# Kernel optimization log

Measured on AMD Instinct MI355X. Metric: run time of the kernel, lower is better.

Reference implementation:

```python
import jax, jax.numpy as jnp
import numpy as np

P_DIMS = [100, 100, 80, 60, 60]
P = sum(P_DIMS)  # 400
N_STREAMS = len(P_DIMS)
MEM_ITERS = 5
DECAY = 0.8
LR = 0.5        # hebbian_learning_rate
FORGET = 0.9999 # hebbian_forget_rate
NEG_SLOPE = 0.01


def _build_masks():
    idx = np.cumsum([0] + P_DIMS)
    hier = np.zeros((P, P), np.float32)
    for i in range(N_STREAMS):
        for j in range(i, N_STREAMS):
            hier[idx[i]:idx[i + 1], idx[j]:idx[j + 1]] = 1.0
    iters = [MEM_ITERS - f for f in range(N_STREAMS)]  # [5,4,3,2,1]
    rmasks = np.zeros((MEM_ITERS, P), np.float32)
    for it in range(MEM_ITERS):
        for s, r in enumerate(iters):
            if it < r:
                rmasks[it, idx[s]:idx[s + 1]] = 1.0
    return jnp.asarray(hier), jnp.asarray(rmasks)


def setup_inputs() -> dict:
    key = jax.random.key(0)
    k1, k2, k3, k4 = jax.random.split(key, 4)
    B = 512
    return {
        'M_prev': jax.random.normal(k1, (B, P, P), dtype=jnp.float32) * 0.1,
        'p_inferred': jax.random.normal(k2, (B, P), dtype=jnp.float32),
        'p_generated': jax.random.normal(k3, (B, P), dtype=jnp.float32),
        'query': jax.random.normal(k4, (B, P), dtype=jnp.float32),
    }


def reference(M_prev, p_inferred, p_generated, query):
    hier_mask, retrieval_masks = _build_masks()

    # Hebbian update: M = clamp(forget*M_prev + lr*(p-phat)(p+phat)^T, -1, 1) * hier_mask
    outer = (p_inferred - p_generated)[:, :, None] * (p_inferred + p_generated)[:, None, :]
    M = jnp.clip(FORGET * M_prev + LR * outer, -1.0, 1.0) * hier_mask

    # Hierarchical attractor retrieval
    h = jax.nn.leaky_relu(jnp.clip(query, -1.0, 1.0), NEG_SLOPE)

    def step(h, mask):
        mv = jnp.einsum('bpq,bq->bp', M, h)
        upd = jax.nn.leaky_relu(jnp.clip(DECAY * h + mv, -1.0, 1.0), NEG_SLOPE)
        return (1.0 - mask) * h + mask * upd, None

    h, _ = jax.lax.scan(step, h, retrieval_masks)
    return h
```

## Files before the change

kernel.cpp:

```cpp
#include <hip/hip_runtime.h>


#define PDIM 400
#define FORGET 0.9999f
#define LRATE  0.5f
#define DECAY  0.8f
#define SLOPE  0.01f

__device__ __forceinline__ float leaky_clip(float x) {
    x = fminf(fmaxf(x, -1.0f), 1.0f);
    return x > 0.0f ? x : SLOPE * x;
}
__device__ __forceinline__ float clamp1(float x) {
    return fminf(fmaxf(x, -1.0f), 1.0f);
}

__device__ __forceinline__ int c4beg(int p) {
    return (p < 100) ? 0 : (p < 200) ? 25 : (p < 280) ? 50 : (p < 340) ? 70 : 85;
}

__device__ __forceinline__ float wave_sum(float x) {
    x += __int_as_float(__builtin_amdgcn_update_dpp(0, __float_as_int(x), 0xB1,  0xf, 0xf, true));
    x += __int_as_float(__builtin_amdgcn_update_dpp(0, __float_as_int(x), 0x4E,  0xf, 0xf, true));
    x += __int_as_float(__builtin_amdgcn_update_dpp(0, __float_as_int(x), 0x141, 0xf, 0xf, true));
    x += __int_as_float(__builtin_amdgcn_update_dpp(0, __float_as_int(x), 0x140, 0xf, 0xf, true));
    x += __int_as_float(__builtin_amdgcn_update_dpp(0, __float_as_int(x), 0x142, 0xf, 0xf, true));
    x += __int_as_float(__builtin_amdgcn_update_dpp(0, __float_as_int(x), 0x143, 0xf, 0xf, true));
    return __int_as_float(__builtin_amdgcn_readlane(__float_as_int(x), 63));
}

__global__ __launch_bounds__(512, 4)
void hier_mem_kernel(const float* __restrict__ M_prev,
                     const float* __restrict__ p_inf,
                     const float* __restrict__ p_gen,
                     const float* __restrict__ query,
                     float* __restrict__ out)
{
    __shared__ float s_h[2][PDIM];
    __shared__ float s_la[PDIM];

    const int b   = blockIdx.x;
    const int tid = threadIdx.x;
    const int l   = tid & 63;
    const int wid = tid >> 6;
    const float* __restrict__ Mb = M_prev + (size_t)b * PDIM * PDIM;

    if (tid < PDIM) {
        const float pi = p_inf[b * PDIM + tid];
        const float pg = p_gen[b * PDIM + tid];
        s_la[tid]   = LRATE * (pi - pg);
        s_h[0][tid] = leaky_clip(query[b * PDIM + tid]);
    }

    const float4 z4 = make_float4(0.f, 0.f, 0.f, 0.f);
    const float4* __restrict__ pi4 = (const float4*)(p_inf + (size_t)b * PDIM);
    const float4* __restrict__ pg4 = (const float4*)(p_gen + (size_t)b * PDIM);
    float4 bA, bB = z4;
    {
        const float4 x = pi4[l], y = pg4[l];
        bA = make_float4(x.x + y.x, x.y + y.y, x.z + y.z, x.w + y.w);
        if (l < 36) {
            const float4 u = pi4[64 + l], v = pg4[64 + l];
            bB = make_float4(u.x + v.x, u.y + v.y, u.z + v.z, u.w + v.w);
        }
    }
    __syncthreads();

    const int Rt[5] = {400, 340, 280, 200, 100};
    int cur = 0;

    #pragma unroll
    for (int t = 0; t < 5; ++t) {
        const int R = Rt[t];
        const float* __restrict__ hcur = s_h[cur];
        float* __restrict__ hnew = s_h[cur ^ 1];

        float4 hA = *(const float4*)(hcur + 4 * l);
        float4 hB = z4;
        if (l < 36) hB = *(const float4*)(hcur + 256 + 4 * l);

        int p = wid;
        int c4 = 0;
        float4 cA = z4, cB = z4;
        if (p < R) {
            c4 = c4beg(p);
            const float* __restrict__ row = Mb + (size_t)p * PDIM;
            if (l >= c4)               cA = *(const float4*)(row + 4 * l);
            if (l < 36 && 64 + l >= c4) cB = *(const float4*)(row + 256 + 4 * l);
        }
        while (p < R) {
            const int pn = p + 8;
            int c4n = 0;
            float4 nA = z4, nB = z4;
            if (pn < R) {
                c4n = c4beg(pn);
                const float* __restrict__ rn = Mb + (size_t)pn * PDIM;
                if (l >= c4n)                nA = *(const float4*)(rn + 4 * l);
                if (l < 36 && 64 + l >= c4n) nB = *(const float4*)(rn + 256 + 4 * l);
            }

            const float la = s_la[p];
            float acc = 0.f;
            if (l >= c4) {
                float m0 = clamp1(fmaf(FORGET, cA.x, la * bA.x));
                float m1 = clamp1(fmaf(FORGET, cA.y, la * bA.y));
                float m2 = clamp1(fmaf(FORGET, cA.z, la * bA.z));
                float m3 = clamp1(fmaf(FORGET, cA.w, la * bA.w));
                acc = fmaf(m0, hA.x, fmaf(m1, hA.y, fmaf(m2, hA.z, m3 * hA.w)));
            }
            if (l < 36 && 64 + l >= c4) {
                float m0 = clamp1(fmaf(FORGET, cB.x, la * bB.x));
                float m1 = clamp1(fmaf(FORGET, cB.y, la * bB.y));
                float m2 = clamp1(fmaf(FORGET, cB.z, la * bB.z));
                float m3 = clamp1(fmaf(FORGET, cB.w, la * bB.w));
                acc = fmaf(m0, hB.x, fmaf(m1, hB.y, fmaf(m2, hB.z, fmaf(m3, hB.w, acc))));
            }

            const float tot = wave_sum(acc);
            if (l == 0) {
                hnew[p] = leaky_clip(fmaf(DECAY, hcur[p], tot));
            }

            p = pn; c4 = c4n; cA = nA; cB = nB;
        }

        if (tid >= R && tid < PDIM) hnew[tid] = hcur[tid];
        __syncthreads();
        cur ^= 1;
    }

    if (tid < PDIM) {
        out[b * PDIM + tid] = s_h[cur][tid];
    }
}

extern "C" void kernel_launch(void* const* d_in, const int* in_sizes, int n_in,
                              void* d_out, int out_size, void* d_ws, size_t ws_size,
                              hipStream_t stream) {
    const float* M_prev = (const float*)d_in[0];
    const float* p_inf  = (const float*)d_in[1];
    const float* p_gen  = (const float*)d_in[2];
    const float* query  = (const float*)d_in[3];
    float* out = (float*)d_out;

    const int B = in_sizes[1] / PDIM;
    hipLaunchKernelGGL(hier_mem_kernel, dim3(B), dim3(512), 0, stream,
                       M_prev, p_inf, p_gen, query, out);
}
```

Baseline: 494.0 us.

## Cache first 96 rows of updated M in LDS and deepen row prefetch

The first 96 rows of the Hebbian-updated memory matrix, which every retrieval iteration reads, are computed once in the first iteration and kept in shared memory. Later iterations read them from LDS instead of reloading from global memory and recomputing the update. Global row loads now prefetch two rows ahead instead of one. The cache takes about 150KB of LDS, so launch bounds drop from 4 to 2 blocks per CU, which costs occupancy.

```diff
diff --git a/kernel.cpp b/kernel.cpp
--- a/kernel.cpp
+++ b/kernel.cpp
@@ -2,6 +2,7 @@
 
 
 #define PDIM 400
+#define CROWS 96
 #define FORGET 0.9999f
 #define LRATE  0.5f
 #define DECAY  0.8f
@@ -29,13 +30,27 @@
     return __int_as_float(__builtin_amdgcn_readlane(__float_as_int(x), 63));
 }
 
-__global__ __launch_bounds__(512, 4)
+__device__ __forceinline__ void load_row(const float* __restrict__ Mb,
+                                         int p, int R, int l,
+                                         int& c4, float4& A, float4& B) {
+    const float4 z4 = make_float4(0.f, 0.f, 0.f, 0.f);
+    c4 = 0; A = z4; B = z4;
+    if (p < R) {
+        c4 = c4beg(p);
+        const float* __restrict__ row = Mb + (size_t)p * PDIM;
+        if (l >= c4)                A = *(const float4*)(row + 4 * l);
+        if (l < 36 && 64 + l >= c4) B = *(const float4*)(row + 256 + 4 * l);
+    }
+}
+
+__global__ __launch_bounds__(512, 2)
 void hier_mem_kernel(const float* __restrict__ M_prev,
                      const float* __restrict__ p_inf,
                      const float* __restrict__ p_gen,
                      const float* __restrict__ query,
                      float* __restrict__ out)
 {
+    __shared__ float s_mc[CROWS][PDIM];
     __shared__ float s_h[2][PDIM];
     __shared__ float s_la[PDIM];
 
@@ -55,22 +70,69 @@
     const float4 z4 = make_float4(0.f, 0.f, 0.f, 0.f);
     const float4* __restrict__ pi4 = (const float4*)(p_inf + (size_t)b * PDIM);
     const float4* __restrict__ pg4 = (const float4*)(p_gen + (size_t)b * PDIM);
-    float4 bA, bB = z4;
+    float4 vA, vB = z4;
     {
         const float4 x = pi4[l], y = pg4[l];
-        bA = make_float4(x.x + y.x, x.y + y.y, x.z + y.z, x.w + y.w);
+        vA = make_float4(x.x + y.x, x.y + y.y, x.z + y.z, x.w + y.w);
         if (l < 36) {
             const float4 u = pi4[64 + l], v = pg4[64 + l];
-            bB = make_float4(u.x + v.x, u.y + v.y, u.z + v.z, u.w + v.w);
+            vB = make_float4(u.x + v.x, u.y + v.y, u.z + v.z, u.w + v.w);
         }
     }
     __syncthreads();
 
-    const int Rt[5] = {400, 340, 280, 200, 100};
-    int cur = 0;
-
+    {
+        const float* __restrict__ hcur = s_h[0];
+        float* __restrict__ hnew = s_h[1];
+        float4 hA = *(const float4*)(hcur + 4 * l);
+        float4 hB = z4;
+        if (l < 36) hB = *(const float4*)(hcur + 256 + 4 * l);
+
+        int p = wid;
+        int c0, c1; float4 A0, B0, A1, B1;
+        load_row(Mb, p,     PDIM, l, c0, A0, B0);
+        load_row(Mb, p + 8, PDIM, l, c1, A1, B1);
+
+        while (p < PDIM) {
+            int c2; float4 A2, B2;
+            load_row(Mb, p + 16, PDIM, l, c2, A2, B2);
+
+            const float la = s_la[p];
+            float acc = 0.f;
+            float4 mA = z4, mB = z4;
+            if (l >= c0) {
+                mA.x = clamp1(fmaf(FORGET, A0.x, la * vA.x));
+                mA.y = clamp1(fmaf(FORGET, A0.y, la * vA.y));
+                mA.z = clamp1(fmaf(FORGET, A0.z, la * vA.z));
+                mA.w = clamp1(fmaf(FORGET, A0.w, la * vA.w));
+                acc = fmaf(mA.x, hA.x, fmaf(mA.y, hA.y, fmaf(mA.z, hA.z, mA.w * hA.w)));
+            }
+            if (l < 36 && 64 + l >= c0) {
+                mB.x = clamp1(fmaf(FORGET, B0.x, la * vB.x));
+                mB.y = clamp1(fmaf(FORGET, B0.y, la * vB.y));
+                mB.z = clamp1(fmaf(FORGET, B0.z, la * vB.z));
+                mB.w = clamp1(fmaf(FORGET, B0.w, la * vB.w));
+                acc = fmaf(mB.x, hB.x, fmaf(mB.y, hB.y, fmaf(mB.z, hB.z, fmaf(mB.w, hB.w, acc))));
+            }
+            if (p < CROWS) {
+                *(float4*)&s_mc[p][4 * l] = mA;
+                if (l < 36) *(float4*)&s_mc[p][256 + 4 * l] = mB;
+            }
+
+            const float tot = wave_sum(acc);
+            if (l == 0) {
+                hnew[p] = leaky_clip(fmaf(DECAY, hcur[p], tot));
+            }
+
+            p += 8; c0 = c1; A0 = A1; B0 = B1; c1 = c2; A1 = A2; B1 = B2;
+        }
+        __syncthreads();
+    }
+
+    int cur = 1;
+    const int Rt[4] = {340, 280, 200, 100};
     #pragma unroll
-    for (int t = 0; t < 5; ++t) {
+    for (int t = 0; t < 4; ++t) {
         const int R = Rt[t];
         const float* __restrict__ hcur = s_h[cur];
         float* __restrict__ hnew = s_h[cur ^ 1];
@@ -79,49 +141,60 @@
         float4 hB = z4;
         if (l < 36) hB = *(const float4*)(hcur + 256 + 4 * l);
 
-        int p = wid;
-        int c4 = 0;
-        float4 cA = z4, cB = z4;
-        if (p < R) {
-            c4 = c4beg(p);
-            const float* __restrict__ row = Mb + (size_t)p * PDIM;
-            if (l >= c4)               cA = *(const float4*)(row + 4 * l);
-            if (l < 36 && 64 + l >= c4) cB = *(const float4*)(row + 256 + 4 * l);
-        }
-        while (p < R) {
-            const int pn = p + 8;
-            int c4n = 0;
-            float4 nA = z4, nB = z4;
-            if (pn < R) {
-                c4n = c4beg(pn);
-                const float* __restrict__ rn = Mb + (size_t)pn * PDIM;
-                if (l >= c4n)                nA = *(const float4*)(rn + 4 * l);
-                if (l < 36 && 64 + l >= c4n) nB = *(const float4*)(rn + 256 + 4 * l);
-            }
-
-            const float la = s_la[p];
+        int sp = CROWS + wid;
+        int c0, c1; float4 A0, B0, A1, B1;
+        load_row(Mb, sp,     R, l, c0, A0, B0);
+        load_row(Mb, sp + 8, R, l, c1, A1, B1);
+
+        {
+            int p = wid;
+            float4 KA = *(const float4*)&s_mc[p][4 * l];
+            float4 KB = z4;
+            if (l < 36) KB = *(const float4*)&s_mc[p][256 + 4 * l];
+            while (p < CROWS) {
+                const int pn = p + 8;
+                float4 NA = z4, NB = z4;
+                if (pn < CROWS) {
+                    NA = *(const float4*)&s_mc[pn][4 * l];
+                    if (l < 36) NB = *(const float4*)&s_mc[pn][256 + 4 * l];
+                }
+                float acc = fmaf(KA.x, hA.x, fmaf(KA.y, hA.y, fmaf(KA.z, hA.z, KA.w * hA.w)));
+                acc = fmaf(KB.x, hB.x, fmaf(KB.y, hB.y, fmaf(KB.z, hB.z, fmaf(KB.w, hB.w, acc))));
+                const float tot = wave_sum(acc);
+                if (l == 0) {
+                    hnew[p] = leaky_clip(fmaf(DECAY, hcur[p], tot));
+                }
+                p = pn; KA = NA; KB = NB;
+            }
+        }
+
+        while (sp < R) {
+            int c2; float4 A2, B2;
+            load_row(Mb, sp + 16, R, l, c2, A2, B2);
+
+            const float la = s_la[sp];
             float acc = 0.f;
-            if (l >= c4) {
-                float m0 = clamp1(fmaf(FORGET, cA.x, la * bA.x));
-                float m1 = clamp1(fmaf(FORGET, cA.y, la * bA.y));
-                float m2 = clamp1(fmaf(FORGET, cA.z, la * bA.z));
-                float m3 = clamp1(fmaf(FORGET, cA.w, la * bA.w));
+            if (l >= c0) {
+                float m0 = clamp1(fmaf(FORGET, A0.x, la * vA.x));
+                float m1 = clamp1(fmaf(FORGET, A0.y, la * vA.y));
+                float m2 = clamp1(fmaf(FORGET, A0.z, la * vA.z));
+                float m3 = clamp1(fmaf(FORGET, A0.w, la * vA.w));
                 acc = fmaf(m0, hA.x, fmaf(m1, hA.y, fmaf(m2, hA.z, m3 * hA.w)));
             }
-            if (l < 36 && 64 + l >= c4) {
-                float m0 = clamp1(fmaf(FORGET, cB.x, la * bB.x));
-                float m1 = clamp1(fmaf(FORGET, cB.y, la * bB.y));
-                float m2 = clamp1(fmaf(FORGET, cB.z, la * bB.z));
-                float m3 = clamp1(fmaf(FORGET, cB.w, la * bB.w));
+            if (l < 36 && 64 + l >= c0) {
+                float m0 = clamp1(fmaf(FORGET, B0.x, la * vB.x));
+                float m1 = clamp1(fmaf(FORGET, B0.y, la * vB.y));
+                float m2 = clamp1(fmaf(FORGET, B0.z, la * vB.z));
+                float m3 = clamp1(fmaf(FORGET, B0.w, la * vB.w));
                 acc = fmaf(m0, hB.x, fmaf(m1, hB.y, fmaf(m2, hB.z, fmaf(m3, hB.w, acc))));
             }
 
             const float tot = wave_sum(acc);
             if (l == 0) {
-                hnew[p] = leaky_clip(fmaf(DECAY, hcur[p], tot));
-            }
-
-            p = pn; c4 = c4n; cA = nA; cB = nB;
+                hnew[sp] = leaky_clip(fmaf(DECAY, hcur[sp], tot));
+            }
+
+            sp += 8; c0 = c1; A0 = A1; B0 = B1; c1 = c2; A1 = A2; B1 = B2;
         }
 
         if (tid >= R && tid < PDIM) hnew[tid] = hcur[tid];
```

Measured after the change: 503.7 us. About the same (+2.0%).
